# Kernel tuning notes

Measured on AMD Instinct MI355X. Metric: run time of the kernel, lower is better.

The kernel has to match this reference:

```python
import jax, jax.numpy as jnp
import numpy as np

EPS_FEAT = 1.0 + 1e-4   # feature_map offset: elu(x) + 1.0 + 0.0001
EPS_DEN = 1e-6


def setup_inputs() -> dict:
    key = jax.random.key(0)
    k1, k2, k3 = jax.random.split(key, 3)
    B, L, D = 4, 4096, 1024
    x = jax.random.normal(k1, (B, L, D), dtype=jnp.float32)
    # torch Linear-style init scale ~ 1/sqrt(fan_in)
    W_qkv = jax.random.normal(k2, (D, 3 * D), dtype=jnp.float32) / np.sqrt(D)
    b_qkv = jnp.zeros((3 * D,), dtype=jnp.float32)
    W_out = jax.random.normal(k3, (D, D), dtype=jnp.float32) / np.sqrt(D)
    b_out = jnp.zeros((D,), dtype=jnp.float32)
    return {"x": x, "W_qkv": W_qkv, "b_qkv": b_qkv, "W_out": W_out, "b_out": b_out}


def _linear_attention(x, W_qkv, b_qkv, W_out, b_out, num_heads=16):
    B, L, D = x.shape
    H = num_heads
    E = D // H

    qkv = x @ W_qkv + b_qkv                       # (B, L, 3D)
    q, k, v = jnp.split(qkv, 3, axis=-1)
    q = q.reshape(B, L, H, E)
    k = k.reshape(B, L, H, E)
    v = v.reshape(B, L, H, E)

    q = jax.nn.elu(q * (E ** -0.5)) + EPS_FEAT    # scale BEFORE feature map (as in source)
    k = jax.nn.elu(k) + EPS_FEAT

    # Causal linear attention via recurrence over L; math identical to
    # cumsum of k \otimes v outer products, but never materializes (B,L,H,E,E).
    qL = jnp.moveaxis(q, 1, 0)                    # (L, B, H, E)
    kL = jnp.moveaxis(k, 1, 0)
    vL = jnp.moveaxis(v, 1, 0)

    kv0 = jnp.zeros((B, H, E, E), dtype=x.dtype)
    ks0 = jnp.zeros((B, H, E), dtype=x.dtype)

    def step(carry, qkv_t):
        kv_s, k_s = carry
        q_t, k_t, v_t = qkv_t                     # each (B, H, E)
        kv_s = kv_s + jnp.einsum('bhe,bhf->bhef', k_t, v_t)
        k_s = k_s + k_t
        num = jnp.einsum('bhe,bhef->bhf', q_t, kv_s)           # (B, H, E)
        den = jnp.einsum('bhe,bhe->bh', q_t, k_s)[..., None] + EPS_DEN
        return (kv_s, k_s), num / den

    _, out = jax.lax.scan(step, (kv0, ks0), (qL, kL, vL))       # out: (L, B, H, E)
    out = jnp.moveaxis(out, 0, 1).reshape(B, L, D)
    # dropout is identity in eval mode
    return out @ W_out + b_out


def reference(x, W_qkv, b_qkv, W_out, b_out):
    return _linear_attention(x, W_qkv, b_qkv, W_out, b_out)
```

## Files before the change

kernel.cpp:

```cpp
#include <hip/hip_runtime.h>
#include <hip/hip_bf16.h>
#include <stdint.h>

#define B_ 4
#define L_ 4096
#define D_ 1024
#define H_ 16
#define E_ 64
#define M_ (B_*L_)
#define N1_ (3*D_)
#define CHK 128
#define NC (L_/CHK)
#define BH (B_*H_)

#define EPS_FEAT 1.0001f
#define EPS_DEN 1e-6f

typedef __attribute__((ext_vector_type(4))) float f32x4;
typedef __attribute__((ext_vector_type(8))) short bf16x8;

__device__ __forceinline__ unsigned short f2bf(float x) {
    union { float f; unsigned int u; } v; v.f = x;
    unsigned int r = v.u + 0x7FFFu + ((v.u >> 16) & 1u);
    return (unsigned short)(r >> 16);
}

__device__ __forceinline__ void gload_lds16(const unsigned short* g, unsigned short* l) {
    __builtin_amdgcn_global_load_lds(
        (const __attribute__((address_space(1))) unsigned int*)(const void*)g,
        (__attribute__((address_space(3))) unsigned int*)(void*)l,
        16, 0, 0);
}


__global__ __launch_bounds__(256) void cvt_x(const float* __restrict__ x,
                                             unsigned short* __restrict__ xb) {
    int i4 = blockIdx.x * 256 + threadIdx.x;
    float4 v = ((const float4*)x)[i4];
    unsigned int lo = (unsigned int)f2bf(v.x) | ((unsigned int)f2bf(v.y) << 16);
    unsigned int hi = (unsigned int)f2bf(v.z) | ((unsigned int)f2bf(v.w) << 16);
    ((uint2*)xb)[i4] = make_uint2(lo, hi);
}

__global__ __launch_bounds__(256) void transp_w2(const float* __restrict__ W0,
                                                 const float* __restrict__ W1,
                                                 unsigned short* __restrict__ T0,
                                                 unsigned short* __restrict__ T1) {
    int z = blockIdx.z;
    if (z == 1 && blockIdx.x >= (D_ / 32)) return;
    const float* W = z ? W1 : W0;
    unsigned short* WT = z ? T1 : T0;
    int N = z ? D_ : N1_;
    __shared__ float tile[32][33];
    int kb = blockIdx.y * 32, nb = blockIdx.x * 32;
    int tx = threadIdx.x & 31, ty = threadIdx.x >> 5;
#pragma unroll
    for (int j = 0; j < 4; ++j)
        tile[ty + 8*j][tx] = W[(size_t)(kb + ty + 8*j) * N + nb + tx];
    __syncthreads();
#pragma unroll
    for (int j = 0; j < 4; ++j) {
        int nl = ty + 8*j;
        WT[(size_t)(nb + nl) * D_ + kb + tx] = f2bf(tile[tx][nl]);
    }
}


template<int MODE, int KDIM, int NDIM>
__global__ __launch_bounds__(512, 2) void gemm256(
    const unsigned short* __restrict__ A,
    const unsigned short* __restrict__ BT,
    const float* __restrict__ bias,
    float* __restrict__ outF,
    unsigned short* __restrict__ qf,
    unsigned short* __restrict__ kf,
    unsigned short* __restrict__ vf)
{
    __shared__ __align__(16) unsigned short smem[65536];

    const int t = threadIdx.x, lane = t & 63, w = t >> 6;
    const int wr = w >> 2, wc = w & 3;

    const int nwgx = NDIM / 256;
    const int nwg = nwgx * (M_ / 256);
    const int bid0 = blockIdx.y * nwgx + blockIdx.x;
    const int swz = (bid0 & 7) * (nwg >> 3) + (bid0 >> 3);
    const int m0 = (swz / nwgx) * 256, n0 = (swz % nwgx) * 256;
    const int lr = lane & 15, lg = lane >> 4;

    auto stage = [&](int T, int ab, int h) {
        unsigned short* base = smem + (T & 1) * 32768 + ab * 16384 + h * 8192;
        const unsigned short* src = ab ? BT : A;
        const int boff = (ab ? n0 : m0) + h * 128;
        const int kt = T * 64;
#pragma unroll
        for (int i = 0; i < 2; ++i) {
            int c = i * 512 + t;
            int rowl = c >> 3, s = c & 7;
            int col = ((s ^ (rowl & 7)) << 3);
            gload_lds16(src + (size_t)(boff + rowl) * KDIM + kt + col, &base[c * 8]);
        }
    };

    bf16x8 af[4][2], bq[4][2];
    f32x4 acc[8][4] = {};

    auto rdA = [&](const unsigned short* Ab, int m, int ks) {
        int row = wr * 128 + m * 16 + lr;
        int slot = (ks * 4 + lg) ^ (row & 7);
        return *(const bf16x8*)&Ab[row * 64 + slot * 8];
    };
    auto rdB = [&](const unsigned short* Bb, int n, int ks) {
        int row = wc * 64 + n * 16 + lr;
        int slot = (ks * 4 + lg) ^ (row & 7);
        return *(const bf16x8*)&Bb[row * 64 + slot * 8];
    };

#define PHASE_PRE() \
    __builtin_amdgcn_s_barrier(); \
    asm volatile("s_waitcnt lgkmcnt(0)" ::: "memory"); \
    __builtin_amdgcn_sched_barrier(0); \
    __builtin_amdgcn_s_setprio(1);
#define PHASE_POST() \
    __builtin_amdgcn_s_setprio(0);

    auto tile = [&](int T, bool s1, bool s2) {
        const unsigned short* Ab = smem + (T & 1) * 32768;
        const unsigned short* Bb = Ab + 16384;
#pragma unroll
        for (int m = 0; m < 4; ++m) { af[m][0] = rdA(Ab, m, 0); af[m][1] = rdA(Ab, m, 1); }
#pragma unroll
        for (int j = 0; j < 2; ++j) { bq[j][0] = rdB(Bb, j, 0); bq[j][1] = rdB(Bb, j, 1); }
        if (s1) stage(T + 1, 0, 0);
        PHASE_PRE();
#pragma unroll
        for (int m = 0; m < 4; ++m)
#pragma unroll
            for (int j = 0; j < 2; ++j) {
                acc[m][j] = __builtin_amdgcn_mfma_f32_16x16x32_bf16(af[m][0], bq[j][0], acc[m][j], 0, 0, 0);
                acc[m][j] = __builtin_amdgcn_mfma_f32_16x16x32_bf16(af[m][1], bq[j][1], acc[m][j], 0, 0, 0);
            }
        PHASE_POST();
#pragma unroll
        for (int j = 0; j < 2; ++j) { bq[2+j][0] = rdB(Bb, 2+j, 0); bq[2+j][1] = rdB(Bb, 2+j, 1); }
        if (s1) stage(T + 1, 0, 1);
        PHASE_PRE();
#pragma unroll
        for (int m = 0; m < 4; ++m)
#pragma unroll
            for (int j = 0; j < 2; ++j) {
                acc[m][2+j] = __builtin_amdgcn_mfma_f32_16x16x32_bf16(af[m][0], bq[2+j][0], acc[m][2+j], 0, 0, 0);
                acc[m][2+j] = __builtin_amdgcn_mfma_f32_16x16x32_bf16(af[m][1], bq[2+j][1], acc[m][2+j], 0, 0, 0);
            }
        PHASE_POST();
#pragma unroll
        for (int m = 0; m < 4; ++m) { af[m][0] = rdA(Ab, 4+m, 0); af[m][1] = rdA(Ab, 4+m, 1); }
        PHASE_PRE();
#pragma unroll
        for (int m = 0; m < 4; ++m)
#pragma unroll
            for (int j = 0; j < 2; ++j) {
                acc[4+m][j] = __builtin_amdgcn_mfma_f32_16x16x32_bf16(af[m][0], bq[j][0], acc[4+m][j], 0, 0, 0);
                acc[4+m][j] = __builtin_amdgcn_mfma_f32_16x16x32_bf16(af[m][1], bq[j][1], acc[4+m][j], 0, 0, 0);
            }
        PHASE_POST();
        if (s2) { stage(T + 2, 1, 0); stage(T + 2, 1, 1); }
        PHASE_PRE();
#pragma unroll
        for (int m = 0; m < 4; ++m)
#pragma unroll
            for (int j = 0; j < 2; ++j) {
                acc[4+m][2+j] = __builtin_amdgcn_mfma_f32_16x16x32_bf16(af[m][0], bq[2+j][0], acc[4+m][2+j], 0, 0, 0);
                acc[4+m][2+j] = __builtin_amdgcn_mfma_f32_16x16x32_bf16(af[m][1], bq[2+j][1], acc[4+m][2+j], 0, 0, 0);
            }
        PHASE_POST();
    };

    constexpr int NT = KDIM / 64;
    stage(0, 0, 0); stage(0, 0, 1); stage(0, 1, 0); stage(0, 1, 1);
    stage(1, 1, 0); stage(1, 1, 1);
    asm volatile("s_waitcnt vmcnt(4)" ::: "memory");
    __builtin_amdgcn_s_barrier();
    __builtin_amdgcn_sched_barrier(0);

    for (int T = 0; T < NT - 2; ++T) {
        tile(T, true, true);
        asm volatile("s_waitcnt vmcnt(4)" ::: "memory");
        __builtin_amdgcn_s_barrier();
        __builtin_amdgcn_sched_barrier(0);
    }
    tile(NT - 2, true, false);
    asm volatile("s_waitcnt vmcnt(0)" ::: "memory");
    __builtin_amdgcn_s_barrier();
    __builtin_amdgcn_sched_barrier(0);
    tile(NT - 1, false, false);
    __syncthreads();

    if (MODE == 0) {
        unsigned short* cbf = smem;
        const bool isQ = (n0 < D_), isK = (n0 >= D_ && n0 < 2*D_);
        const float scale = isQ ? 0.125f : 1.0f;
        unsigned short* buf = isQ ? qf : (isK ? kf : vf);
        const int b = m0 >> 12, l0 = m0 & 4095;
        const int h0 = (n0 & 1023) >> 6;
#pragma unroll
        for (int p = 0; p < 2; ++p) {
            if (wr == p) {
#pragma unroll
                for (int n = 0; n < 4; ++n) {
                    int cl = wc*64 + n*16 + lr;
                    float bv = bias[n0 + cl];
#pragma unroll
                    for (int m = 0; m < 8; ++m)
#pragma unroll
                        for (int q = 0; q < 4; ++q) {
                            int rl = m*16 + lg*4 + q;
                            float val = (acc[m][n][q] + bv) * scale;
                            float fv = (isQ || isK)
                                       ? ((val > 0.f ? val : __expf(val) - 1.f) + EPS_FEAT)
                                       : val;
                            cbf[rl * 264 + cl] = f2bf(fv);
                        }
                }
            }
            __syncthreads();
#pragma unroll
            for (int hh = 0; hh < 4; ++hh) {
                unsigned short* dst = buf + (((size_t)(b * H_ + h0 + hh)) * L_ + l0 + p*128) * E_;
#pragma unroll
                for (int i = 0; i < 2; ++i) {
                    int c = i*512 + t, row = c >> 3, ch = c & 7;
                    uint4 v = *(const uint4*)&cbf[row * 264 + hh*64 + ch*8];
                    *(uint4*)&dst[row * 64 + ch*8] = v;
                }
            }
            __syncthreads();
        }
    } else {
        float* cfl = (float*)smem;
#pragma unroll
        for (int p = 0; p < 4; ++p) {
            if (wr == (p >> 1)) {
                int mbase = (p & 1) * 4;
#pragma unroll
                for (int n = 0; n < 4; ++n) {
                    int cl = wc*64 + n*16 + lr;
                    float bv = bias[n0 + cl];
#pragma unroll
                    for (int mm = 0; mm < 4; ++mm)
#pragma unroll
                        for (int q = 0; q < 4; ++q) {
                            int rl = mm*16 + lg*4 + q;
                            cfl[rl * 260 + cl] = acc[mbase + mm][n][q] + bv;
                        }
                }
            }
            __syncthreads();
#pragma unroll
            for (int i = 0; i < 8; ++i) {
                int c = i*512 + t, row = c >> 6, ch = c & 63;
                float4 v = *(const float4*)&cfl[row * 260 + ch*4];
                *(float4*)&outF[(size_t)(m0 + p*64 + row) * NDIM + n0 + ch*4] = v;
            }
            __syncthreads();
        }
    }
#undef PHASE_PRE
#undef PHASE_POST
}


__global__ __launch_bounds__(256) void chunk_kv(
    const unsigned short* __restrict__ kf, const unsigned short* __restrict__ vf,
    float* __restrict__ kvout, float* __restrict__ ksout)
{
    constexpr int LDK = 136;
    __shared__ unsigned short Kt[64 * LDK];
    __shared__ unsigned short Vt[80 * LDK];

    int t = threadIdx.x, lane = t & 63, w = t >> 6;
    int bid = blockIdx.x;
    const unsigned short* kp = kf + (size_t)bid * CHK * E_;
    const unsigned short* vp = vf + (size_t)bid * CHK * E_;

#pragma unroll
    for (int it = 0; it < 4; ++it) {
        int s = it * 256 + t;
        int rl = s >> 3, e0 = (s & 7) << 3;
        uint4 kv8 = *(const uint4*)(kp + s * 8);
        uint4 vv8 = *(const uint4*)(vp + s * 8);
        unsigned int kw[4] = {kv8.x, kv8.y, kv8.z, kv8.w};
        unsigned int vw[4] = {vv8.x, vv8.y, vv8.z, vv8.w};
#pragma unroll
        for (int jw = 0; jw < 4; ++jw) {
            Kt[(e0 + 2*jw    ) * LDK + rl] = (unsigned short)(kw[jw] & 0xFFFF);
            Kt[(e0 + 2*jw + 1) * LDK + rl] = (unsigned short)(kw[jw] >> 16);
            Vt[(e0 + 2*jw    ) * LDK + rl] = (unsigned short)(vw[jw] & 0xFFFF);
            Vt[(e0 + 2*jw + 1) * LDK + rl] = (unsigned short)(vw[jw] >> 16);
        }
    }
    if (t < 128) Vt[64 * LDK + t] = 0x3F80;
    for (int i = t; i < 15 * LDK; i += 256) Vt[65 * LDK + i] = 0;
    __syncthreads();

    int lr = lane & 15, lg = lane >> 4;
    f32x4 acc[4] = {};
    f32x4 accE[4] = {};
#pragma unroll
    for (int ks = 0; ks < 4; ++ks) {
        bf16x8 a = *(const bf16x8*)&Vt[(w*16 + lr) * LDK + ks*32 + lg*8];
#pragma unroll
        for (int n = 0; n < 4; ++n) {
            bf16x8 b = *(const bf16x8*)&Kt[(n*16 + lr) * LDK + ks*32 + lg*8];
            acc[n] = __builtin_amdgcn_mfma_f32_16x16x32_bf16(a, b, acc[n], 0, 0, 0);
        }
    }
    if (w == 0) {
#pragma unroll
        for (int ks = 0; ks < 4; ++ks) {
            bf16x8 a = *(const bf16x8*)&Vt[(64 + lr) * LDK + ks*32 + lg*8];
#pragma unroll
            for (int n = 0; n < 4; ++n) {
                bf16x8 b = *(const bf16x8*)&Kt[(n*16 + lr) * LDK + ks*32 + lg*8];
                accE[n] = __builtin_amdgcn_mfma_f32_16x16x32_bf16(a, b, accE[n], 0, 0, 0);
            }
        }
    }
    float* kvo = kvout + (size_t)bid * E_ * E_;
#pragma unroll
    for (int n = 0; n < 4; ++n)
#pragma unroll
        for (int q = 0; q < 4; ++q) {
            int f = w*16 + lg*4 + q, e = n*16 + lr;
            kvo[f * 64 + e] = acc[n][q];
        }
    if (w == 0 && lg == 0) {
#pragma unroll
        for (int n = 0; n < 4; ++n)
            ksout[(size_t)bid * 64 + n*16 + lr] = accE[n][0];
    }
}


__global__ __launch_bounds__(256) void prefix_kv(
    const float* __restrict__ kv, const float* __restrict__ ks,
    unsigned short* __restrict__ kvb, unsigned short* __restrict__ ksb)
{
    int bh = blockIdx.y, part = blockIdx.x, t = threadIdx.x;
    int idx = part * 256 + t;
    float st = 0.f;
    for (int c = 0; c < NC; ++c) {
        float tmp = kv[((size_t)bh * NC + c) * 4096 + idx];
        kvb[((size_t)bh * NC + c) * 4096 + idx] = f2bf(st);
        st += tmp;
    }
    if (part == 0 && t < 64) {
        float s0 = 0.f;
        for (int c = 0; c < NC; ++c) {
            float tmp = ks[((size_t)bh * NC + c) * 64 + t];
            ksb[((size_t)bh * NC + c) * 64 + t] = f2bf(s0);
            s0 += tmp;
        }
    }
}


__global__ __launch_bounds__(256, 2) void attn_out(
    const unsigned short* __restrict__ qf, const unsigned short* __restrict__ kf,
    const unsigned short* __restrict__ vf, const unsigned short* __restrict__ kvb,
    const unsigned short* __restrict__ ksb, unsigned short* __restrict__ attn)
{
    constexpr int LK = 72;
    constexpr int LV = 136;
    __shared__ unsigned short Ks[128 * LK];
    __shared__ unsigned short Vt[64 * LV];
    __shared__ unsigned short Ss[128 * LV];

    int t = threadIdx.x, lane = t & 63, w = t >> 6;
    int bid = blockIdx.x;
    int bh = bid >> 5, c = bid & 31;
    const unsigned short* qp = qf + (size_t)bid * CHK * E_;
    const unsigned short* kp = kf + (size_t)bid * CHK * E_;
    const unsigned short* vp = vf + (size_t)bid * CHK * E_;
    const unsigned short* kvp = kvb + (size_t)bid * 4096;

    int lr = lane & 15, lg = lane >> 4;
    const int jsel[2] = {w, 7 - w};

    bf16x8 aq[2][2];
#pragma unroll
    for (int mi = 0; mi < 2; ++mi)
#pragma unroll
        for (int ks = 0; ks < 2; ++ks)
            aq[mi][ks] = *(const bf16x8*)(qp + (jsel[mi]*16 + lr) * 64 + ks*32 + lg*8);

#pragma unroll
    for (int it = 0; it < 4; ++it) {
        int s = it * 256 + t;
        int r = s >> 3, e0 = (s & 7) << 3;
        uint4 kv = *(const uint4*)(kp + s * 8);
        uint4 vv = *(const uint4*)(vp + s * 8);
        *(uint4*)&Ks[r * LK + e0] = kv;
        unsigned int vw[4] = {vv.x, vv.y, vv.z, vv.w};
#pragma unroll
        for (int jw = 0; jw < 4; ++jw) {
            Vt[(e0 + 2*jw    ) * LV + r] = (unsigned short)(vw[jw] & 0xFFFF);
            Vt[(e0 + 2*jw + 1) * LV + r] = (unsigned short)(vw[jw] >> 16);
        }
    }
    bf16x8 zfrag = {0,0,0,0,0,0,0,0};
    bf16x8 bone = zfrag, bks[2] = {zfrag, zfrag};
    if (lr == 0) {
#pragma unroll
        for (int j = 0; j < 8; ++j) bone[j] = (short)0x3F80;
        bks[0] = *(const bf16x8*)&ksb[(size_t)bid * 64 + lg*8];
        bks[1] = *(const bf16x8*)&ksb[(size_t)bid * 64 + 32 + lg*8];
    }
    __syncthreads();

#pragma unroll
    for (int mi = 0; mi < 2; ++mi) {
        int j = jsel[mi];
        int rbase = j * 16;
        int jbmax = j | 1;
        for (int jb = 0; jb <= jbmax; ++jb) {
            if (jb <= j) {
                f32x4 sacc = {};
                bf16x8 b0 = *(const bf16x8*)&Ks[(jb*16 + lr) * LK + lg*8];
                bf16x8 b1 = *(const bf16x8*)&Ks[(jb*16 + lr) * LK + 32 + lg*8];
                sacc = __builtin_amdgcn_mfma_f32_16x16x32_bf16(aq[mi][0], b0, sacc, 0, 0, 0);
                sacc = __builtin_amdgcn_mfma_f32_16x16x32_bf16(aq[mi][1], b1, sacc, 0, 0, 0);
#pragma unroll
                for (int q = 0; q < 4; ++q) {
                    int r = rbase + lg*4 + q;
                    int jj = jb*16 + lr;
                    Ss[r * LV + jj] = (jj <= r) ? f2bf(sacc[q]) : (unsigned short)0;
                }
            } else {
#pragma unroll
                for (int q = 0; q < 4; ++q) {
                    int r = rbase + lg*4 + q;
                    Ss[r * LV + jb*16 + lr] = 0;
                }
            }
        }
    }

    f32x4 oacc[2][5] = {};
#pragma unroll
    for (int mi = 0; mi < 2; ++mi) {
        int j = jsel[mi];
        int rbase = j * 16;
#pragma unroll
        for (int ks = 0; ks < 2; ++ks) {
            bf16x8 a = aq[mi][ks];
#pragma unroll
            for (int n = 0; n < 4; ++n) {
                bf16x8 b = *(const bf16x8*)&kvp[(n*16 + lr) * 64 + ks*32 + lg*8];
                oacc[mi][n] = __builtin_amdgcn_mfma_f32_16x16x32_bf16(a, b, oacc[mi][n], 0, 0, 0);
            }
            oacc[mi][4] = __builtin_amdgcn_mfma_f32_16x16x32_bf16(a, bks[ks], oacc[mi][4], 0, 0, 0);
        }
        for (int ks = 0; ks <= (j >> 1); ++ks) {
            bf16x8 a = *(const bf16x8*)&Ss[(rbase + lr) * LV + ks*32 + lg*8];
#pragma unroll
            for (int n = 0; n < 4; ++n) {
                bf16x8 b = *(const bf16x8*)&Vt[(n*16 + lr) * LV + ks*32 + lg*8];
                oacc[mi][n] = __builtin_amdgcn_mfma_f32_16x16x32_bf16(a, b, oacc[mi][n], 0, 0, 0);
            }
            oacc[mi][4] = __builtin_amdgcn_mfma_f32_16x16x32_bf16(a, bone, oacc[mi][4], 0, 0, 0);
        }
    }

    int b_idx = bh >> 4, h_idx = bh & 15;
#pragma unroll
    for (int mi = 0; mi < 2; ++mi) {
        int rbase = jsel[mi] * 16;
        float den[4];
#pragma unroll
        for (int q = 0; q < 4; ++q)
            den[q] = __shfl(oacc[mi][4][q], lane & 48, 64) + EPS_DEN;
#pragma unroll
        for (int n = 0; n < 4; ++n) {
#pragma unroll
            for (int q = 0; q < 4; ++q) {
                int r = rbase + lg*4 + q;
                int lpos = c * CHK + r;
                int col = n*16 + lr;
                size_t dst = ((size_t)b_idx * L_ + lpos) * D_ + h_idx * 64 + col;
                attn[dst] = f2bf(oacc[mi][n][q] / den[q]);
            }
        }
    }
}


extern "C" void kernel_launch(void* const* d_in, const int* in_sizes, int n_in,
                              void* d_out, int out_size, void* d_ws, size_t ws_size,
                              hipStream_t stream)
{
    const float* x    = (const float*)d_in[0];
    const float* Wqkv = (const float*)d_in[1];
    const float* bqkv = (const float*)d_in[2];
    const float* Wout = (const float*)d_in[3];
    const float* bout = (const float*)d_in[4];
    float* out = (float*)d_out;

    char* ws = (char*)d_ws;
    size_t off = 0;
    auto alloc = [&](size_t bytes) { void* p = ws + off; off += (bytes + 255) & ~(size_t)255; return p; };
    unsigned short* xb  = (unsigned short*)alloc((size_t)M_ * D_ * 2);
    unsigned short* WqT = (unsigned short*)alloc((size_t)N1_ * D_ * 2);
    unsigned short* WoT = (unsigned short*)alloc((size_t)D_ * D_ * 2);
    unsigned short* qfb = (unsigned short*)alloc((size_t)M_ * D_ * 2);
    unsigned short* kfb = (unsigned short*)alloc((size_t)M_ * D_ * 2);
    unsigned short* vfb = (unsigned short*)alloc((size_t)M_ * D_ * 2);
    float* kvw = (float*)alloc((size_t)BH * NC * E_ * E_ * 4);
    float* ksw = (float*)alloc((size_t)BH * NC * E_ * 4);
    unsigned short* kvb = (unsigned short*)alloc((size_t)BH * NC * E_ * E_ * 2);
    unsigned short* ksb = (unsigned short*)alloc((size_t)BH * NC * E_ * 2);
    unsigned short* attn = xb;

    cvt_x<<<(M_ * D_ / 4) / 256, 256, 0, stream>>>(x, xb);
    transp_w2<<<dim3(N1_ / 32, D_ / 32, 2), 256, 0, stream>>>(Wqkv, Wout, WqT, WoT);

    gemm256<0, D_, N1_><<<dim3(N1_ / 256, M_ / 256), 512, 0, stream>>>(
        xb, WqT, bqkv, nullptr, qfb, kfb, vfb);

    chunk_kv<<<BH * NC, 256, 0, stream>>>(kfb, vfb, kvw, ksw);
    prefix_kv<<<dim3(16, BH), 256, 0, stream>>>(kvw, ksw, kvb, ksb);
    attn_out<<<BH * NC, 256, 0, stream>>>(qfb, kfb, vfb, kvb, ksb, attn);

    gemm256<1, D_, D_><<<dim3(D_ / 256, M_ / 256), 512, 0, stream>>>(
        attn, WoT, bout, out, nullptr, nullptr, nullptr);
}
```

Measured before the change: 242.1 us.

## Merge prep kernels, restructure GEMM inner tile into two phases, vectorize prefix scan

Folds the x-to-bf16 conversion and both weight transposes into one launch to cut launch overhead. The GEMM tile body now runs two MFMA phases instead of four: it loads all four B fragments and a full A half up front and issues both A-stage loads together. This raises register pressure and reduces the overlap between LDS reads and MFMAs. The prefix_kv scan now handles float4 per thread with a quarter of the blocks, which gives wider memory accesses but less parallelism.

After: 239.9 us. About the same (-0.9%).

```diff
diff --git a/kernel.cpp b/kernel.cpp
--- a/kernel.cpp
+++ b/kernel.cpp
@@ -33,27 +33,33 @@
 }
 
 
-__global__ __launch_bounds__(256) void cvt_x(const float* __restrict__ x,
-                                             unsigned short* __restrict__ xb) {
-    int i4 = blockIdx.x * 256 + threadIdx.x;
-    float4 v = ((const float4*)x)[i4];
-    unsigned int lo = (unsigned int)f2bf(v.x) | ((unsigned int)f2bf(v.y) << 16);
-    unsigned int hi = (unsigned int)f2bf(v.z) | ((unsigned int)f2bf(v.w) << 16);
-    ((uint2*)xb)[i4] = make_uint2(lo, hi);
-}
-
-__global__ __launch_bounds__(256) void transp_w2(const float* __restrict__ W0,
-                                                 const float* __restrict__ W1,
-                                                 unsigned short* __restrict__ T0,
-                                                 unsigned short* __restrict__ T1) {
-    int z = blockIdx.z;
-    if (z == 1 && blockIdx.x >= (D_ / 32)) return;
-    const float* W = z ? W1 : W0;
-    unsigned short* WT = z ? T1 : T0;
-    int N = z ? D_ : N1_;
+__global__ __launch_bounds__(256) void prep(const float* __restrict__ x,
+                                            const float* __restrict__ W0,
+                                            const float* __restrict__ W1,
+                                            unsigned short* __restrict__ xb,
+                                            unsigned short* __restrict__ T0,
+                                            unsigned short* __restrict__ T1) {
     __shared__ float tile[32][33];
-    int kb = blockIdx.y * 32, nb = blockIdx.x * 32;
-    int tx = threadIdx.x & 31, ty = threadIdx.x >> 5;
+    int bid = blockIdx.x, t = threadIdx.x;
+    if (bid < 16384) {
+        int i4 = bid * 256 + t;
+        float4 v = ((const float4*)x)[i4];
+        unsigned int lo = (unsigned int)f2bf(v.x) | ((unsigned int)f2bf(v.y) << 16);
+        unsigned int hi = (unsigned int)f2bf(v.z) | ((unsigned int)f2bf(v.w) << 16);
+        ((uint2*)xb)[i4] = make_uint2(lo, hi);
+        return;
+    }
+    const float* W; unsigned short* WT; int N, nb, kb;
+    if (bid < 16384 + 3072) {
+        int idx = bid - 16384;
+        W = W0; WT = T0; N = N1_;
+        nb = (idx % 96) * 32; kb = (idx / 96) * 32;
+    } else {
+        int idx = bid - 16384 - 3072;
+        W = W1; WT = T1; N = D_;
+        nb = (idx % 32) * 32; kb = (idx / 32) * 32;
+    }
+    int tx = t & 31, ty = t >> 5;
 #pragma unroll
     for (int j = 0; j < 4; ++j)
         tile[ty + 8*j][tx] = W[(size_t)(kb + ty + 8*j) * N + nb + tx];
@@ -102,7 +108,6 @@
         }
     };
 
-    bf16x8 af[4][2], bq[4][2];
     f32x4 acc[8][4] = {};
 
     auto rdA = [&](const unsigned short* Ab, int m, int ks) {
@@ -127,51 +132,31 @@
     auto tile = [&](int T, bool s1, bool s2) {
         const unsigned short* Ab = smem + (T & 1) * 32768;
         const unsigned short* Bb = Ab + 16384;
-#pragma unroll
-        for (int m = 0; m < 4; ++m) { af[m][0] = rdA(Ab, m, 0); af[m][1] = rdA(Ab, m, 1); }
-#pragma unroll
-        for (int j = 0; j < 2; ++j) { bq[j][0] = rdB(Bb, j, 0); bq[j][1] = rdB(Bb, j, 1); }
-        if (s1) stage(T + 1, 0, 0);
+        bf16x8 a0[4][2], a1[4][2], bq[4][2];
+#pragma unroll
+        for (int m = 0; m < 4; ++m) { a0[m][0] = rdA(Ab, m, 0); a0[m][1] = rdA(Ab, m, 1); }
+#pragma unroll
+        for (int n = 0; n < 4; ++n) { bq[n][0] = rdB(Bb, n, 0); bq[n][1] = rdB(Bb, n, 1); }
+        if (s1) { stage(T + 1, 0, 0); stage(T + 1, 0, 1); }
         PHASE_PRE();
 #pragma unroll
         for (int m = 0; m < 4; ++m)
 #pragma unroll
-            for (int j = 0; j < 2; ++j) {
-                acc[m][j] = __builtin_amdgcn_mfma_f32_16x16x32_bf16(af[m][0], bq[j][0], acc[m][j], 0, 0, 0);
-                acc[m][j] = __builtin_amdgcn_mfma_f32_16x16x32_bf16(af[m][1], bq[j][1], acc[m][j], 0, 0, 0);
+            for (int n = 0; n < 4; ++n) {
+                acc[m][n] = __builtin_amdgcn_mfma_f32_16x16x32_bf16(a0[m][0], bq[n][0], acc[m][n], 0, 0, 0);
+                acc[m][n] = __builtin_amdgcn_mfma_f32_16x16x32_bf16(a0[m][1], bq[n][1], acc[m][n], 0, 0, 0);
             }
         PHASE_POST();
 #pragma unroll
-        for (int j = 0; j < 2; ++j) { bq[2+j][0] = rdB(Bb, 2+j, 0); bq[2+j][1] = rdB(Bb, 2+j, 1); }
-        if (s1) stage(T + 1, 0, 1);
-        PHASE_PRE();
-#pragma unroll
-        for (int m = 0; m < 4; ++m)
-#pragma unroll
-            for (int j = 0; j < 2; ++j) {
-                acc[m][2+j] = __builtin_amdgcn_mfma_f32_16x16x32_bf16(af[m][0], bq[2+j][0], acc[m][2+j], 0, 0, 0);
-                acc[m][2+j] = __builtin_amdgcn_mfma_f32_16x16x32_bf16(af[m][1], bq[2+j][1], acc[m][2+j], 0, 0, 0);
-            }
-        PHASE_POST();
-#pragma unroll
-        for (int m = 0; m < 4; ++m) { af[m][0] = rdA(Ab, 4+m, 0); af[m][1] = rdA(Ab, 4+m, 1); }
-        PHASE_PRE();
-#pragma unroll
-        for (int m = 0; m < 4; ++m)
-#pragma unroll
-            for (int j = 0; j < 2; ++j) {
-                acc[4+m][j] = __builtin_amdgcn_mfma_f32_16x16x32_bf16(af[m][0], bq[j][0], acc[4+m][j], 0, 0, 0);
-                acc[4+m][j] = __builtin_amdgcn_mfma_f32_16x16x32_bf16(af[m][1], bq[j][1], acc[4+m][j], 0, 0, 0);
-            }
-        PHASE_POST();
+        for (int m = 0; m < 4; ++m) { a1[m][0] = rdA(Ab, 4+m, 0); a1[m][1] = rdA(Ab, 4+m, 1); }
         if (s2) { stage(T + 2, 1, 0); stage(T + 2, 1, 1); }
         PHASE_PRE();
 #pragma unroll
         for (int m = 0; m < 4; ++m)
 #pragma unroll
-            for (int j = 0; j < 2; ++j) {
-                acc[4+m][2+j] = __builtin_amdgcn_mfma_f32_16x16x32_bf16(af[m][0], bq[2+j][0], acc[4+m][2+j], 0, 0, 0);
-                acc[4+m][2+j] = __builtin_amdgcn_mfma_f32_16x16x32_bf16(af[m][1], bq[2+j][1], acc[4+m][2+j], 0, 0, 0);
+            for (int n = 0; n < 4; ++n) {
+                acc[4+m][n] = __builtin_amdgcn_mfma_f32_16x16x32_bf16(a1[m][0], bq[n][0], acc[4+m][n], 0, 0, 0);
+                acc[4+m][n] = __builtin_amdgcn_mfma_f32_16x16x32_bf16(a1[m][1], bq[n][1], acc[4+m][n], 0, 0, 0);
             }
         PHASE_POST();
     };
@@ -343,16 +328,18 @@
 
 
 __global__ __launch_bounds__(256) void prefix_kv(
-    const float* __restrict__ kv, const float* __restrict__ ks,
-    unsigned short* __restrict__ kvb, unsigned short* __restrict__ ksb)
+    const float4* __restrict__ kv, const float* __restrict__ ks,
+    uint2* __restrict__ kvb, unsigned short* __restrict__ ksb)
 {
     int bh = blockIdx.y, part = blockIdx.x, t = threadIdx.x;
     int idx = part * 256 + t;
-    float st = 0.f;
+    float4 st = make_float4(0.f, 0.f, 0.f, 0.f);
     for (int c = 0; c < NC; ++c) {
-        float tmp = kv[((size_t)bh * NC + c) * 4096 + idx];
-        kvb[((size_t)bh * NC + c) * 4096 + idx] = f2bf(st);
-        st += tmp;
+        float4 tmp = kv[((size_t)bh * NC + c) * 1024 + idx];
+        kvb[((size_t)bh * NC + c) * 1024 + idx] = make_uint2(
+            (unsigned int)f2bf(st.x) | ((unsigned int)f2bf(st.y) << 16),
+            (unsigned int)f2bf(st.z) | ((unsigned int)f2bf(st.w) << 16));
+        st.x += tmp.x; st.y += tmp.y; st.z += tmp.z; st.w += tmp.w;
     }
     if (part == 0 && t < 64) {
         float s0 = 0.f;
@@ -521,14 +508,13 @@
     unsigned short* ksb = (unsigned short*)alloc((size_t)BH * NC * E_ * 2);
     unsigned short* attn = xb;
 
-    cvt_x<<<(M_ * D_ / 4) / 256, 256, 0, stream>>>(x, xb);
-    transp_w2<<<dim3(N1_ / 32, D_ / 32, 2), 256, 0, stream>>>(Wqkv, Wout, WqT, WoT);
+    prep<<<16384 + 3072 + 1024, 256, 0, stream>>>(x, Wqkv, Wout, xb, WqT, WoT);
 
     gemm256<0, D_, N1_><<<dim3(N1_ / 256, M_ / 256), 512, 0, stream>>>(
         xb, WqT, bqkv, nullptr, qfb, kfb, vfb);
 
     chunk_kv<<<BH * NC, 256, 0, stream>>>(kfb, vfb, kvw, ksw);
-    prefix_kv<<<dim3(16, BH), 256, 0, stream>>>(kvw, ksw, kvb, ksb);
+    prefix_kv<<<dim3(4, BH), 256, 0, stream>>>((const float4*)kvw, ksw, (uint2*)kvb, ksb);
     attn_out<<<BH * NC, 256, 0, stream>>>(qfb, kfb, vfb, kvb, ksb, attn);
 
     gemm256<1, D_, D_><<<dim3(D_ / 256, M_ / 256), 512, 0, stream>>>(
```
